# Optimization experiments

Hardware: AMD Instinct MI355X
Metric: run time of the kernel (lower is better)

Reference implementation:

```python
import jax, jax.numpy as jnp
import numpy as np

N = 100000   # nodes
DEG = 4      # fixed out-degree (>2 so every node survives the c>2 mask)
E = N * DEG  # edges
IN = 128
H = 256


def _lin_params(key, fan_out, fan_in, bias=True):
    k1, k2 = jax.random.split(key)
    W = 0.05 * jax.random.normal(k1, (fan_out, fan_in), jnp.float32)
    if bias:
        b = 0.05 * jax.random.normal(k2, (fan_out,), jnp.float32)
        return W, b
    return W


def setup_inputs() -> dict:
    key = jax.random.key(0)
    ks = jax.random.split(key, 12)
    x = jax.random.normal(ks[0], (N, IN), jnp.float32)
    # every node has exactly DEG outgoing edges -> out-degree 4 > 2 for all nodes
    src = jnp.repeat(jnp.arange(N, dtype=jnp.int32), DEG)
    dst = jax.random.randint(ks[1], (E,), 0, N, dtype=jnp.int32)
    edge_index = jnp.stack([src, dst])  # [2, E]
    batch = jnp.zeros((N,), jnp.int32)
    Wr0, br0 = _lin_params(ks[2], H, IN)
    Ws0 = _lin_params(ks[3], H, IN, bias=False)
    Wr1, br1 = _lin_params(ks[4], H, H)
    Ws1 = _lin_params(ks[5], H, H, bias=False)
    Wr2, br2 = _lin_params(ks[6], H, H)
    Ws2 = _lin_params(ks[7], H, H, bias=False)
    Wsp1, bsp1 = _lin_params(ks[8], 1, H)
    Wsp2, bsp2 = _lin_params(ks[9], 1, H)
    Wl, bl = _lin_params(ks[10], 1, 2)
    return dict(x=x, edge_index=edge_index, batch=batch,
                Wr0=Wr0, br0=br0, Ws0=Ws0,
                Wr1=Wr1, br1=br1, Ws1=Ws1,
                Wr2=Wr2, br2=br2, Ws2=Ws2,
                Wsp1=Wsp1, bsp1=bsp1, Wsp2=Wsp2, bsp2=bsp2,
                Wl=Wl, bl=bl)


def reference(x, edge_index, batch, Wr0, br0, Ws0, Wr1, br1, Ws1,
              Wr2, br2, Ws2, Wsp1, bsp1, Wsp2, bsp2, Wl, bl):
    src, dst = edge_index[0], edge_index[1]

    def gconv(h, Wr, br, Ws):
        # PyG GraphConv(aggr='add'): out_i = W_rel @ sum_{j->i} h_j + b + W_root @ h_i
        agg = jax.ops.segment_sum(h[src], dst, num_segments=N)
        return jax.nn.relu(agg @ Wr.T + br + h @ Ws.T)

    h = gconv(x, Wr0, br0, Ws0)
    h = gconv(h, Wr1, br1, Ws1)
    h = gconv(h, Wr2, br2, Ws2)

    # unique(edge_index[0], counts) ; keep source nodes with out-degree > 2
    deg = jax.ops.segment_sum(jnp.ones((E,), h.dtype), src, num_segments=N)
    sel = jnp.nonzero(deg > 2, size=N, fill_value=0)[0]  # all N nodes by construction
    xs = h[sel].reshape(-1, 2 * H)  # pair consecutive nodes
    x1, x2 = xs[:, :H], xs[:, H:]
    out = jnp.concatenate([jax.nn.relu(x1 @ Wsp1.T + bsp1),
                           jax.nn.relu(x2 @ Wsp2.T + bsp2)], axis=1)
    y = jax.nn.sigmoid(out @ Wl.T + bl)  # split=True branch
    return y, xs, x1, x2
```

## Files before the change

### kernel.cpp

```cpp
#include <hip/hip_runtime.h>
#include <hip/hip_bf16.h>
#include <math.h>

#define NNODES 100000
#define NEDGES 400000
#define INDIM  128
#define HDIM   256
#define MAXDEG 32

#define BM 64
#define BN 256
#define BK 64
#define MTILES 1563

typedef __attribute__((ext_vector_type(8))) short short8;
typedef __attribute__((ext_vector_type(8))) unsigned short ushort8v;
typedef __attribute__((ext_vector_type(4))) float f32x4;

__device__ __forceinline__ float bf2f(unsigned short u) {
    union { unsigned int i; float f; } v; v.i = ((unsigned int)u) << 16; return v.f;
}
__device__ __forceinline__ unsigned short f2bf(float f) {
    union { float f; unsigned int i; } v; v.f = f;
    unsigned int r = v.i + 0x7fffu + ((v.i >> 16) & 1u);
    return (unsigned short)(r >> 16);
}

__device__ __forceinline__ void async_load16(const void* g, void* l) {
    __builtin_amdgcn_global_load_lds(
        (const __attribute__((address_space(1))) unsigned int*)g,
        (__attribute__((address_space(3))) unsigned int*)l,
        16, 0, 0);
}

#define XB_BLOCKS 12500
#define W0_BLOCKS 256
#define W1_BLOCKS 512
#define EL_BLOCKS 1563
#define PREP_BLOCKS (XB_BLOCKS + W0_BLOCKS + 2 * W1_BLOCKS + EL_BLOCKS)

__global__ void prep_kernel(const float* __restrict__ x, unsigned short* __restrict__ xb,
                            const float* __restrict__ Wr0, const float* __restrict__ Ws0,
                            unsigned short* __restrict__ B0,
                            const float* __restrict__ Wr1, const float* __restrict__ Ws1,
                            unsigned short* __restrict__ B1,
                            const float* __restrict__ Wr2, const float* __restrict__ Ws2,
                            unsigned short* __restrict__ B2,
                            const int* __restrict__ ei, int* __restrict__ cnt,
                            int* __restrict__ elist) {
    int b = blockIdx.x;
    if (b < XB_BLOCKS) {
        int i = b * 256 + threadIdx.x;
        float4 v = ((const float4*)x)[i];
        ushort4 o; o.x = f2bf(v.x); o.y = f2bf(v.y); o.z = f2bf(v.z); o.w = f2bf(v.w);
        ((ushort4*)xb)[i] = o;
        return;
    }
    b -= XB_BLOCKS;
    if (b < W0_BLOCKS + 2 * W1_BLOCKS) {
        const float *Wr, *Ws; unsigned short* B; int K;
        if (b < W0_BLOCKS)               { Wr = Wr0; Ws = Ws0; B = B0; K = INDIM; }
        else if (b < W0_BLOCKS + W1_BLOCKS) { Wr = Wr1; Ws = Ws1; B = B1; K = HDIM; b -= W0_BLOCKS; }
        else                              { Wr = Wr2; Ws = Ws2; B = B2; K = HDIM; b -= W0_BLOCKS + W1_BLOCKS; }
        int idx = b * 256 + threadIdx.x;
        int n = idx / (2 * K);
        int k = idx - n * 2 * K;
        float v = (k < K) ? Wr[n * K + k] : Ws[n * K + (k - K)];
        B[idx] = f2bf(v);
        return;
    }
    b -= W0_BLOCKS + 2 * W1_BLOCKS;
    int e = b * 256 + threadIdx.x;
    if (e < NEDGES) {
        int d = ei[NEDGES + e];
        int s = ei[e];
        int pos = atomicAdd(&cnt[d], 1);
        if (pos < MAXDEG) elist[d * MAXDEG + pos] = s;
    }
}

__global__ void gather_bf16_128(const unsigned short* __restrict__ h, const int* __restrict__ cnt,
                                const int* __restrict__ elist, unsigned short* __restrict__ agg) {
    int wid  = (blockIdx.x * blockDim.x + threadIdx.x) >> 6;
    int lane = threadIdx.x & 63;
    if (wid >= NNODES) return;
    int c = cnt[wid]; if (c > MAXDEG) c = MAXDEG;
    const int4* el4 = (const int4*)(elist + wid * MAXDEG);
    float a0 = 0.f, a1 = 0.f;
    for (int j0 = 0; j0 < c; j0 += 4) {
        int4 e = el4[j0 >> 2];
        int rem = c - j0;
        ushort2 v0 = {0,0}, v1 = {0,0}, v2 = {0,0}, v3 = {0,0};
        v0 = ((const ushort2*)(h + (size_t)e.x * INDIM))[lane];
        if (rem > 1) v1 = ((const ushort2*)(h + (size_t)e.y * INDIM))[lane];
        if (rem > 2) v2 = ((const ushort2*)(h + (size_t)e.z * INDIM))[lane];
        if (rem > 3) v3 = ((const ushort2*)(h + (size_t)e.w * INDIM))[lane];
        a0 += bf2f(v0.x) + bf2f(v1.x) + bf2f(v2.x) + bf2f(v3.x);
        a1 += bf2f(v0.y) + bf2f(v1.y) + bf2f(v2.y) + bf2f(v3.y);
    }
    ushort2 o; o.x = f2bf(a0); o.y = f2bf(a1);
    ((ushort2*)(agg + (size_t)wid * INDIM))[lane] = o;
}

__global__ void gather_bf16_256(const unsigned short* __restrict__ h, const int* __restrict__ cnt,
                                const int* __restrict__ elist, unsigned short* __restrict__ agg) {
    int wid  = (blockIdx.x * blockDim.x + threadIdx.x) >> 6;
    int lane = threadIdx.x & 63;
    if (wid >= NNODES) return;
    int c = cnt[wid]; if (c > MAXDEG) c = MAXDEG;
    const int4* el4 = (const int4*)(elist + wid * MAXDEG);
    float a0 = 0.f, a1 = 0.f, a2 = 0.f, a3 = 0.f;
    for (int j0 = 0; j0 < c; j0 += 4) {
        int4 e = el4[j0 >> 2];
        int rem = c - j0;
        ushort4 v0 = {0,0,0,0}, v1 = {0,0,0,0}, v2 = {0,0,0,0}, v3 = {0,0,0,0};
        v0 = ((const ushort4*)(h + (size_t)e.x * HDIM))[lane];
        if (rem > 1) v1 = ((const ushort4*)(h + (size_t)e.y * HDIM))[lane];
        if (rem > 2) v2 = ((const ushort4*)(h + (size_t)e.z * HDIM))[lane];
        if (rem > 3) v3 = ((const ushort4*)(h + (size_t)e.w * HDIM))[lane];
        a0 += bf2f(v0.x) + bf2f(v1.x) + bf2f(v2.x) + bf2f(v3.x);
        a1 += bf2f(v0.y) + bf2f(v1.y) + bf2f(v2.y) + bf2f(v3.y);
        a2 += bf2f(v0.z) + bf2f(v1.z) + bf2f(v2.z) + bf2f(v3.z);
        a3 += bf2f(v0.w) + bf2f(v1.w) + bf2f(v2.w) + bf2f(v3.w);
    }
    ushort4 o; o.x = f2bf(a0); o.y = f2bf(a1); o.z = f2bf(a2); o.w = f2bf(a3);
    ((ushort4*)(agg + (size_t)wid * HDIM))[lane] = o;
}

template<int MODE>
__global__ __launch_bounds__(256)
void gemm_kernel(const unsigned short* __restrict__ A1, const unsigned short* __restrict__ A2,
                 int K, const unsigned short* __restrict__ B, const float* __restrict__ bias,
                 unsigned short* __restrict__ hout,
                 float* __restrict__ xs, float* __restrict__ x1o, float* __restrict__ x2o,
                 const float* __restrict__ Wsp1, const float* __restrict__ Wsp2,
                 float* __restrict__ spart) {
    __shared__ __align__(16) unsigned char smem[(BM * BK + BN * BK) * 2];
    unsigned short* Ash = (unsigned short*)smem;
    unsigned short* Bsh = Ash + BM * BK;

    const int tid  = threadIdx.x;
    const int lane = tid & 63;
    const int wn   = tid >> 6;
    const int m0   = blockIdx.x * BM;
    const int Ktot = 2 * K;

    f32x4 acc[4][4];
    for (int i = 0; i < 4; i++)
        for (int j = 0; j < 4; j++)
            acc[i][j] = (f32x4){0.f, 0.f, 0.f, 0.f};

    for (int k0 = 0; k0 < Ktot; k0 += BK) {
        const unsigned short* Abase; int koff;
        if (k0 < K) { Abase = A1; koff = k0; } else { Abase = A2; koff = k0 - K; }

        #pragma unroll
        for (int it = 0; it < 2; it++) {
            int idx = it * 256 + tid;
            int row = idx >> 3, seg = idx & 7;
            int gseg = seg ^ (row & 7);
            int grow = m0 + row; if (grow >= NNODES) grow = NNODES - 1;
            async_load16(Abase + (size_t)grow * K + koff + gseg * 8, &Ash[idx * 8]);
        }
        #pragma unroll
        for (int it = 0; it < 8; it++) {
            int idx = it * 256 + tid;
            int row = idx >> 3, seg = idx & 7;
            int gseg = seg ^ (row & 7);
            async_load16(B + (size_t)row * Ktot + k0 + gseg * 8, &Bsh[idx * 8]);
        }
        __syncthreads();

        #pragma unroll
        for (int half = 0; half < 2; half++) {
            short8 af[4], bfr[4];
            #pragma unroll
            for (int mt = 0; mt < 4; mt++) {
                int ml  = mt * 16 + (lane & 15);
                int seg = half * 4 + (lane >> 4);
                int ps  = seg ^ (ml & 7);
                af[mt] = *(const short8*)&Ash[ml * BK + ps * 8];
            }
            #pragma unroll
            for (int nt = 0; nt < 4; nt++) {
                int nl  = wn * 64 + nt * 16 + (lane & 15);
                int seg = half * 4 + (lane >> 4);
                int ps  = seg ^ (nl & 7);
                bfr[nt] = *(const short8*)&Bsh[nl * BK + ps * 8];
            }
            #pragma unroll
            for (int mt = 0; mt < 4; mt++)
                #pragma unroll
                for (int nt = 0; nt < 4; nt++)
                    acc[mt][nt] = __builtin_amdgcn_mfma_f32_16x16x32_bf16(
                        af[mt], bfr[nt], acc[mt][nt], 0, 0, 0);
        }
        __syncthreads();
    }

    float* bounce = (float*)smem;
    float* wb = bounce + wn * (16 * 68);
    const int q    = lane & 3;
    const int rrow = lane >> 2;

    #pragma unroll
    for (int mt = 0; mt < 4; mt++) {
        __syncthreads();
        #pragma unroll
        for (int nt = 0; nt < 4; nt++)
            #pragma unroll
            for (int rr = 0; rr < 4; rr++)
                wb[((lane >> 4) * 4 + rr) * 68 + nt * 16 + (lane & 15)] = acc[mt][nt][rr];
        __syncthreads();

        int grow = m0 + mt * 16 + rrow;
        int gc   = wn * 64 + q * 16;
        float4 v[4];
        #pragma unroll
        for (int s = 0; s < 4; s++)
            v[s] = ((const float4*)(wb + rrow * 68 + q * 16))[s];

        if (grow < NNODES) {
            const float4* bv = (const float4*)(bias + gc);
            #pragma unroll
            for (int s = 0; s < 4; s++) {
                float4 b4 = bv[s];
                v[s].x = fmaxf(v[s].x + b4.x, 0.f);
                v[s].y = fmaxf(v[s].y + b4.y, 0.f);
                v[s].z = fmaxf(v[s].z + b4.z, 0.f);
                v[s].w = fmaxf(v[s].w + b4.w, 0.f);
            }
            if (MODE == 0) {
                ushort8v o0, o1;
                o0[0]=f2bf(v[0].x); o0[1]=f2bf(v[0].y); o0[2]=f2bf(v[0].z); o0[3]=f2bf(v[0].w);
                o0[4]=f2bf(v[1].x); o0[5]=f2bf(v[1].y); o0[6]=f2bf(v[1].z); o0[7]=f2bf(v[1].w);
                o1[0]=f2bf(v[2].x); o1[1]=f2bf(v[2].y); o1[2]=f2bf(v[2].z); o1[3]=f2bf(v[2].w);
                o1[4]=f2bf(v[3].x); o1[5]=f2bf(v[3].y); o1[6]=f2bf(v[3].z); o1[7]=f2bf(v[3].w);
                ushort8v* dst = (ushort8v*)(hout + (size_t)grow * HDIM + gc);
                dst[0] = o0; dst[1] = o1;
            } else {
                float4* xsp = (float4*)(xs + (size_t)grow * HDIM + gc);
                #pragma unroll
                for (int s = 0; s < 4; s++) xsp[s] = v[s];
                float* xo = (grow & 1) ? x2o : x1o;
                float4* xop = (float4*)(xo + (size_t)(grow >> 1) * HDIM + gc);
                #pragma unroll
                for (int s = 0; s < 4; s++) xop[s] = v[s];
                const float* wsp = (grow & 1) ? Wsp2 : Wsp1;
                const float4* wv = (const float4*)(wsp + gc);
                float p = 0.f;
                #pragma unroll
                for (int s = 0; s < 4; s++) {
                    float4 w4 = wv[s];
                    p += v[s].x * w4.x + v[s].y * w4.y + v[s].z * w4.z + v[s].w * w4.w;
                }
                p += __shfl_xor(p, 1);
                p += __shfl_xor(p, 2);
                if (q == 0) atomicAdd(&spart[grow], p);
            }
        }
    }
}

__global__ void finalize_kernel(const float* __restrict__ spart, const float* __restrict__ bsp1,
                                const float* __restrict__ bsp2, const float* __restrict__ Wl,
                                const float* __restrict__ bl, float* __restrict__ y) {
    int p = blockIdx.x * 256 + threadIdx.x;
    if (p < NNODES / 2) {
        float s1 = spart[2 * p]     + bsp1[0]; s1 = s1 > 0.f ? s1 : 0.f;
        float s2 = spart[2 * p + 1] + bsp2[0]; s2 = s2 > 0.f ? s2 : 0.f;
        float t = s1 * Wl[0] + s2 * Wl[1] + bl[0];
        y[p] = 1.f / (1.f + expf(-t));
    }
}

extern "C" void kernel_launch(void* const* d_in, const int* in_sizes, int n_in,
                              void* d_out, int out_size, void* d_ws, size_t ws_size,
                              hipStream_t stream) {
    const float* x    = (const float*)d_in[0];
    const int*   ei   = (const int*)d_in[1];
    const float* Wr0  = (const float*)d_in[3];
    const float* br0  = (const float*)d_in[4];
    const float* Ws0  = (const float*)d_in[5];
    const float* Wr1  = (const float*)d_in[6];
    const float* br1  = (const float*)d_in[7];
    const float* Ws1  = (const float*)d_in[8];
    const float* Wr2  = (const float*)d_in[9];
    const float* br2  = (const float*)d_in[10];
    const float* Ws2  = (const float*)d_in[11];
    const float* Wsp1 = (const float*)d_in[12];
    const float* bsp1 = (const float*)d_in[13];
    const float* Wsp2 = (const float*)d_in[14];
    const float* bsp2 = (const float*)d_in[15];
    const float* Wl   = (const float*)d_in[16];
    const float* bl   = (const float*)d_in[17];

    char* ws = (char*)d_ws;
    size_t off = 0;
    auto alloc = [&](size_t bytes) -> void* {
        void* p = ws + off;
        off += (bytes + 255) & ~(size_t)255;
        return p;
    };
    int*            cnt   = (int*)alloc((size_t)NNODES * 4);
    float*          spart = (float*)alloc((size_t)NNODES * 4);
    size_t zero_bytes = off;
    int*            elist = (int*)alloc((size_t)NNODES * MAXDEG * 4);
    unsigned short* xb    = (unsigned short*)alloc((size_t)NNODES * INDIM * 2);
    unsigned short* aggb  = (unsigned short*)alloc((size_t)NNODES * HDIM * 2);
    unsigned short* hA    = (unsigned short*)alloc((size_t)NNODES * HDIM * 2);
    unsigned short* hB    = (unsigned short*)alloc((size_t)NNODES * HDIM * 2);
    unsigned short* B0    = (unsigned short*)alloc((size_t)HDIM * 2 * INDIM * 2);
    unsigned short* B1    = (unsigned short*)alloc((size_t)HDIM * 2 * HDIM * 2);
    unsigned short* B2    = (unsigned short*)alloc((size_t)HDIM * 2 * HDIM * 2);

    float* y  = (float*)d_out;
    float* xs = y + 50000;
    float* x1 = xs + (size_t)50000 * 512;
    float* x2 = x1 + (size_t)50000 * 256;

    hipMemsetAsync(ws, 0, zero_bytes, stream);
    prep_kernel<<<PREP_BLOCKS, 256, 0, stream>>>(x, xb, Wr0, Ws0, B0, Wr1, Ws1, B1,
                                                 Wr2, Ws2, B2, ei, cnt, elist);

    int gather_blocks = (NNODES * 64 + 255) / 256;

    gather_bf16_128<<<gather_blocks, 256, 0, stream>>>(xb, cnt, elist, aggb);
    gemm_kernel<0><<<MTILES, 256, 0, stream>>>(aggb, xb, INDIM, B0, br0, hA,
                                               nullptr, nullptr, nullptr,
                                               nullptr, nullptr, nullptr);
    gather_bf16_256<<<gather_blocks, 256, 0, stream>>>(hA, cnt, elist, aggb);
    gemm_kernel<0><<<MTILES, 256, 0, stream>>>(aggb, hA, HDIM, B1, br1, hB,
                                               nullptr, nullptr, nullptr,
                                               nullptr, nullptr, nullptr);
    gather_bf16_256<<<gather_blocks, 256, 0, stream>>>(hB, cnt, elist, aggb);
    gemm_kernel<1><<<MTILES, 256, 0, stream>>>(aggb, hB, HDIM, B2, br2, nullptr,
                                               xs, x1, x2, Wsp1, Wsp2, spart);
    finalize_kernel<<<(NNODES / 2 + 255) / 256, 256, 0, stream>>>(
        spart, bsp1, bsp2, Wl, bl, y);
}
```

Before: 607.1 us.

## Fuse neighbor gather into GEMM kernel via shared-memory aggregate tile

Each GEMM block now aggregates its 64 nodes' neighbor features directly into a swizzled shared-memory tile, then runs the MFMA loop reading the aggregate half of K from LDS and streaming the root half from global. This removes the separate gather kernels and the round-trip of the aggregate buffer through global memory, along with three kernel launches. In exchange, shared memory per block grows (up to about 80KB for K=256), which can reduce occupancy, and the gather phase is serialized before the MFMA work inside each block.

```diff
diff --git a/kernel.cpp b/kernel.cpp
--- a/kernel.cpp
+++ b/kernel.cpp
@@ -79,88 +79,91 @@
     }
 }
 
-__global__ void gather_bf16_128(const unsigned short* __restrict__ h, const int* __restrict__ cnt,
-                                const int* __restrict__ elist, unsigned short* __restrict__ agg) {
-    int wid  = (blockIdx.x * blockDim.x + threadIdx.x) >> 6;
-    int lane = threadIdx.x & 63;
-    if (wid >= NNODES) return;
-    int c = cnt[wid]; if (c > MAXDEG) c = MAXDEG;
-    const int4* el4 = (const int4*)(elist + wid * MAXDEG);
-    float a0 = 0.f, a1 = 0.f;
-    for (int j0 = 0; j0 < c; j0 += 4) {
-        int4 e = el4[j0 >> 2];
-        int rem = c - j0;
-        ushort2 v0 = {0,0}, v1 = {0,0}, v2 = {0,0}, v3 = {0,0};
-        v0 = ((const ushort2*)(h + (size_t)e.x * INDIM))[lane];
-        if (rem > 1) v1 = ((const ushort2*)(h + (size_t)e.y * INDIM))[lane];
-        if (rem > 2) v2 = ((const ushort2*)(h + (size_t)e.z * INDIM))[lane];
-        if (rem > 3) v3 = ((const ushort2*)(h + (size_t)e.w * INDIM))[lane];
-        a0 += bf2f(v0.x) + bf2f(v1.x) + bf2f(v2.x) + bf2f(v3.x);
-        a1 += bf2f(v0.y) + bf2f(v1.y) + bf2f(v2.y) + bf2f(v3.y);
-    }
-    ushort2 o; o.x = f2bf(a0); o.y = f2bf(a1);
-    ((ushort2*)(agg + (size_t)wid * INDIM))[lane] = o;
-}
-
-__global__ void gather_bf16_256(const unsigned short* __restrict__ h, const int* __restrict__ cnt,
-                                const int* __restrict__ elist, unsigned short* __restrict__ agg) {
-    int wid  = (blockIdx.x * blockDim.x + threadIdx.x) >> 6;
-    int lane = threadIdx.x & 63;
-    if (wid >= NNODES) return;
-    int c = cnt[wid]; if (c > MAXDEG) c = MAXDEG;
-    const int4* el4 = (const int4*)(elist + wid * MAXDEG);
-    float a0 = 0.f, a1 = 0.f, a2 = 0.f, a3 = 0.f;
-    for (int j0 = 0; j0 < c; j0 += 4) {
-        int4 e = el4[j0 >> 2];
-        int rem = c - j0;
-        ushort4 v0 = {0,0,0,0}, v1 = {0,0,0,0}, v2 = {0,0,0,0}, v3 = {0,0,0,0};
-        v0 = ((const ushort4*)(h + (size_t)e.x * HDIM))[lane];
-        if (rem > 1) v1 = ((const ushort4*)(h + (size_t)e.y * HDIM))[lane];
-        if (rem > 2) v2 = ((const ushort4*)(h + (size_t)e.z * HDIM))[lane];
-        if (rem > 3) v3 = ((const ushort4*)(h + (size_t)e.w * HDIM))[lane];
-        a0 += bf2f(v0.x) + bf2f(v1.x) + bf2f(v2.x) + bf2f(v3.x);
-        a1 += bf2f(v0.y) + bf2f(v1.y) + bf2f(v2.y) + bf2f(v3.y);
-        a2 += bf2f(v0.z) + bf2f(v1.z) + bf2f(v2.z) + bf2f(v3.z);
-        a3 += bf2f(v0.w) + bf2f(v1.w) + bf2f(v2.w) + bf2f(v3.w);
-    }
-    ushort4 o; o.x = f2bf(a0); o.y = f2bf(a1); o.z = f2bf(a2); o.w = f2bf(a3);
-    ((ushort4*)(agg + (size_t)wid * HDIM))[lane] = o;
-}
-
-template<int MODE>
+template<int KK, int MODE>
 __global__ __launch_bounds__(256)
-void gemm_kernel(const unsigned short* __restrict__ A1, const unsigned short* __restrict__ A2,
-                 int K, const unsigned short* __restrict__ B, const float* __restrict__ bias,
+void fused_layer(const unsigned short* __restrict__ H,
+                 const int* __restrict__ cnt, const int* __restrict__ elist,
+                 const unsigned short* __restrict__ B,
+                 const float* __restrict__ bias,
                  unsigned short* __restrict__ hout,
                  float* __restrict__ xs, float* __restrict__ x1o, float* __restrict__ x2o,
                  const float* __restrict__ Wsp1, const float* __restrict__ Wsp2,
                  float* __restrict__ spart) {
-    __shared__ __align__(16) unsigned char smem[(BM * BK + BN * BK) * 2];
-    unsigned short* Ash = (unsigned short*)smem;
-    unsigned short* Bsh = Ash + BM * BK;
+    __shared__ __align__(16) unsigned char smem[(64 * KK + BN * BK + BM * BK) * 2];
+    unsigned short* Agg = (unsigned short*)smem;
+    unsigned short* Bsh = Agg + 64 * KK;
+    unsigned short* A2  = Bsh + BN * BK;
 
     const int tid  = threadIdx.x;
     const int lane = tid & 63;
     const int wn   = tid >> 6;
     const int m0   = blockIdx.x * BM;
-    const int Ktot = 2 * K;
+    const int Ktot = 2 * KK;
+
+    #pragma unroll 4
+    for (int i = 0; i < 16; i++) {
+        int row  = wn * 16 + i;
+        int node = m0 + row;
+        float a0 = 0.f, a1 = 0.f, a2 = 0.f, a3 = 0.f;
+        if (node < NNODES) {
+            int c = cnt[node]; if (c > MAXDEG) c = MAXDEG;
+            const int4* el4 = (const int4*)(elist + node * MAXDEG);
+            for (int j0 = 0; j0 < c; j0 += 4) {
+                int4 e = el4[j0 >> 2];
+                int rem = c - j0;
+                if constexpr (KK == 256) {
+                    ushort4 v0 = {0,0,0,0}, v1 = {0,0,0,0}, v2 = {0,0,0,0}, v3 = {0,0,0,0};
+                    v0 = ((const ushort4*)(H + (size_t)e.x * KK))[lane];
+                    if (rem > 1) v1 = ((const ushort4*)(H + (size_t)e.y * KK))[lane];
+                    if (rem > 2) v2 = ((const ushort4*)(H + (size_t)e.z * KK))[lane];
+                    if (rem > 3) v3 = ((const ushort4*)(H + (size_t)e.w * KK))[lane];
+                    a0 += bf2f(v0.x) + bf2f(v1.x) + bf2f(v2.x) + bf2f(v3.x);
+                    a1 += bf2f(v0.y) + bf2f(v1.y) + bf2f(v2.y) + bf2f(v3.y);
+                    a2 += bf2f(v0.z) + bf2f(v1.z) + bf2f(v2.z) + bf2f(v3.z);
+                    a3 += bf2f(v0.w) + bf2f(v1.w) + bf2f(v2.w) + bf2f(v3.w);
+                } else {
+                    ushort2 v0 = {0,0}, v1 = {0,0}, v2 = {0,0}, v3 = {0,0};
+                    v0 = ((const ushort2*)(H + (size_t)e.x * KK))[lane];
+                    if (rem > 1) v1 = ((const ushort2*)(H + (size_t)e.y * KK))[lane];
+                    if (rem > 2) v2 = ((const ushort2*)(H + (size_t)e.z * KK))[lane];
+                    if (rem > 3) v3 = ((const ushort2*)(H + (size_t)e.w * KK))[lane];
+                    a0 += bf2f(v0.x) + bf2f(v1.x) + bf2f(v2.x) + bf2f(v3.x);
+                    a1 += bf2f(v0.y) + bf2f(v1.y) + bf2f(v2.y) + bf2f(v3.y);
+                }
+            }
+        }
+        if constexpr (KK == 256) {
+            int s  = lane >> 1;
+            int ps = (s & ~7) | ((s & 7) ^ (row & 7));
+            ushort4 o; o.x = f2bf(a0); o.y = f2bf(a1); o.z = f2bf(a2); o.w = f2bf(a3);
+            *(ushort4*)&Agg[row * KK + ps * 8 + (lane & 1) * 4] = o;
+        } else {
+            int s  = lane >> 2;
+            int ps = (s & ~7) | ((s & 7) ^ (row & 7));
+            ushort2 o; o.x = f2bf(a0); o.y = f2bf(a1);
+            *(ushort2*)&Agg[row * KK + ps * 8 + (lane & 3) * 2] = o;
+        }
+    }
 
     f32x4 acc[4][4];
+    #pragma unroll
     for (int i = 0; i < 4; i++)
+        #pragma unroll
         for (int j = 0; j < 4; j++)
             acc[i][j] = (f32x4){0.f, 0.f, 0.f, 0.f};
 
+    #pragma unroll
     for (int k0 = 0; k0 < Ktot; k0 += BK) {
-        const unsigned short* Abase; int koff;
-        if (k0 < K) { Abase = A1; koff = k0; } else { Abase = A2; koff = k0 - K; }
-
-        #pragma unroll
-        for (int it = 0; it < 2; it++) {
-            int idx = it * 256 + tid;
-            int row = idx >> 3, seg = idx & 7;
-            int gseg = seg ^ (row & 7);
-            int grow = m0 + row; if (grow >= NNODES) grow = NNODES - 1;
-            async_load16(Abase + (size_t)grow * K + koff + gseg * 8, &Ash[idx * 8]);
+        const bool useAgg = (k0 < KK);
+        if (!useAgg) {
+            #pragma unroll
+            for (int it = 0; it < 2; it++) {
+                int idx = it * 256 + tid;
+                int row = idx >> 3, seg = idx & 7;
+                int gseg = seg ^ (row & 7);
+                int grow = m0 + row; if (grow >= NNODES) grow = NNODES - 1;
+                async_load16(H + (size_t)grow * KK + (k0 - KK) + gseg * 8, &A2[idx * 8]);
+            }
         }
         #pragma unroll
         for (int it = 0; it < 8; it++) {
@@ -176,16 +179,21 @@
             short8 af[4], bfr[4];
             #pragma unroll
             for (int mt = 0; mt < 4; mt++) {
-                int ml  = mt * 16 + (lane & 15);
-                int seg = half * 4 + (lane >> 4);
-                int ps  = seg ^ (ml & 7);
-                af[mt] = *(const short8*)&Ash[ml * BK + ps * 8];
+                int ml   = mt * 16 + (lane & 15);
+                int srel = half * 4 + (lane >> 4);
+                if (useAgg) {
+                    int ps = (k0 >> 3) + (srel ^ (ml & 7));
+                    af[mt] = *(const short8*)&Agg[ml * KK + ps * 8];
+                } else {
+                    int ps = srel ^ (ml & 7);
+                    af[mt] = *(const short8*)&A2[ml * BK + ps * 8];
+                }
             }
             #pragma unroll
             for (int nt = 0; nt < 4; nt++) {
-                int nl  = wn * 64 + nt * 16 + (lane & 15);
-                int seg = half * 4 + (lane >> 4);
-                int ps  = seg ^ (nl & 7);
+                int nl   = wn * 64 + nt * 16 + (lane & 15);
+                int srel = half * 4 + (lane >> 4);
+                int ps   = srel ^ (nl & 7);
                 bfr[nt] = *(const short8*)&Bsh[nl * BK + ps * 8];
             }
             #pragma unroll
@@ -307,7 +315,6 @@
     size_t zero_bytes = off;
     int*            elist = (int*)alloc((size_t)NNODES * MAXDEG * 4);
     unsigned short* xb    = (unsigned short*)alloc((size_t)NNODES * INDIM * 2);
-    unsigned short* aggb  = (unsigned short*)alloc((size_t)NNODES * HDIM * 2);
     unsigned short* hA    = (unsigned short*)alloc((size_t)NNODES * HDIM * 2);
     unsigned short* hB    = (unsigned short*)alloc((size_t)NNODES * HDIM * 2);
     unsigned short* B0    = (unsigned short*)alloc((size_t)HDIM * 2 * INDIM * 2);
@@ -323,19 +330,14 @@
     prep_kernel<<<PREP_BLOCKS, 256, 0, stream>>>(x, xb, Wr0, Ws0, B0, Wr1, Ws1, B1,
                                                  Wr2, Ws2, B2, ei, cnt, elist);
 
-    int gather_blocks = (NNODES * 64 + 255) / 256;
-
-    gather_bf16_128<<<gather_blocks, 256, 0, stream>>>(xb, cnt, elist, aggb);
-    gemm_kernel<0><<<MTILES, 256, 0, stream>>>(aggb, xb, INDIM, B0, br0, hA,
-                                               nullptr, nullptr, nullptr,
-                                               nullptr, nullptr, nullptr);
-    gather_bf16_256<<<gather_blocks, 256, 0, stream>>>(hA, cnt, elist, aggb);
-    gemm_kernel<0><<<MTILES, 256, 0, stream>>>(aggb, hA, HDIM, B1, br1, hB,
-                                               nullptr, nullptr, nullptr,
-                                               nullptr, nullptr, nullptr);
-    gather_bf16_256<<<gather_blocks, 256, 0, stream>>>(hB, cnt, elist, aggb);
-    gemm_kernel<1><<<MTILES, 256, 0, stream>>>(aggb, hB, HDIM, B2, br2, nullptr,
-                                               xs, x1, x2, Wsp1, Wsp2, spart);
+    fused_layer<128, 0><<<MTILES, 256, 0, stream>>>(xb, cnt, elist, B0, br0, hA,
+                                                    nullptr, nullptr, nullptr,
+                                                    nullptr, nullptr, nullptr);
+    fused_layer<256, 0><<<MTILES, 256, 0, stream>>>(hA, cnt, elist, B1, br1, hB,
+                                                    nullptr, nullptr, nullptr,
+                                                    nullptr, nullptr, nullptr);
+    fused_layer<256, 1><<<MTILES, 256, 0, stream>>>(hB, cnt, elist, B2, br2, nullptr,
+                                                    xs, x1, x2, Wsp1, Wsp2, spart);
     finalize_kernel<<<(NNODES / 2 + 255) / 256, 256, 0, stream>>>(
         spart, bsp1, bsp2, Wl, bl, y);
 }
```

Result: slower. 829.8 us (+36.7%).
